# Performance work log

Hardware: AMD Instinct MI355X
Metric: run time of the kernel (lower is better)

The kernel has to match this reference:

```python
import jax, jax.numpy as jnp
import numpy as np

B, IN, OUT = 4096, 1024, 1024
HALF_PI = np.pi / 2.0
TWO_PI = 2.0 * np.pi
# cyclic control-point index table per quadrant (from the torch module)
CPI = jnp.array([[3, 0, 1, 2], [0, 1, 2, 3], [1, 2, 3, 0], [2, 3, 0, 1]], dtype=jnp.int32)
# Catmull-Rom cubic spline basis (4 control points, [t^3,t^2,t,1] monomials)
BASIS = np.array([[-0.5, 1.5, -1.5, 0.5],
                  [1.0, -2.5, 2.0, -0.5],
                  [-0.5, 0.0, 0.5, 0.0],
                  [0.0, 1.0, 0.0, 0.0]], dtype=np.float32)


def setup_inputs() -> dict:
    key = jax.random.key(0)
    k_x, k_p, k_w, k_b = jax.random.split(key, 4)
    x = jax.random.normal(k_x, (B, IN), dtype=jnp.float32)
    phase = jax.random.uniform(k_p, (B,), dtype=jnp.float32) * TWO_PI
    # kaiming_uniform_(a=sqrt(5)) on each (OUT, IN) slice -> bound = 1/sqrt(fan_in)
    bound = 1.0 / np.sqrt(IN)
    weights = jax.random.uniform(k_w, (4, OUT, IN), dtype=jnp.float32, minval=-bound, maxval=bound)
    biases = jax.random.uniform(k_b, (4, OUT), dtype=jnp.float32, minval=-bound, maxval=bound)
    basis = jnp.asarray(BASIS)
    return {"input": x, "phase": phase, "weights": weights, "biases": biases, "basis": basis}


def reference(input, phase, weights, biases, basis):
    # quadrant index q in {0,1,2,3}; same selection as the nested torch.where chain
    q = jnp.clip(jnp.floor(phase / HALF_PI).astype(jnp.int32), 0, 3)          # (B,)
    t = phase / HALF_PI - q.astype(phase.dtype)                                # (B,), in [0,1)
    tt = jnp.stack([t ** 3, t ** 2, t, jnp.ones_like(t)], axis=-1)             # (B,4)
    coeffs = tt @ basis                                                        # (B,4) spline coeffs
    idx = CPI[q]                                                               # (B,4) control-point ids
    # Instead of materializing per-sample (B,OUT,IN) weights, contract input against
    # all 4 control-point matrices (same math: w_b = sum_k c_k W_{idx_k}).
    z = jnp.einsum('bi,coi->bco', input, weights)                              # (B,4,OUT)
    zg = jnp.take_along_axis(z, idx[:, :, None], axis=1)                       # (B,4,OUT)
    bg = biases[idx]                                                           # (B,4,OUT)
    return jnp.einsum('bk,bko->bo', coeffs, zg + bg)                           # (B,OUT)
```

## Files before the change

kernel.cpp:

```cpp
#include <hip/hip_runtime.h>
#include <stdint.h>

#define BATCH   4096
#define IN_DIM  1024
#define OUT_DIM 1024

typedef __bf16 bf16x8 __attribute__((ext_vector_type(8)));
typedef float  f32x4  __attribute__((ext_vector_type(4)));

__device__ __forceinline__ uint16_t f2bf(float f) {
    union { float f; uint32_t u; } v; v.f = f;
    uint32_t u = v.u;
    uint32_t r = (u + 0x7FFFu + ((u >> 16) & 1u)) >> 16;
    return (uint16_t)r;
}

__device__ __forceinline__ float bf2f(uint16_t h) {
    union { uint32_t u; float f; } v; v.u = ((uint32_t)h) << 16;
    return v.f;
}

__global__ __launch_bounds__(256) void prep(
    const float* __restrict__ x, const float* __restrict__ phase,
    const float* __restrict__ basis, const float* __restrict__ W,
    uint16_t* __restrict__ xb, uint16_t* __restrict__ Wb,
    float* __restrict__ alphaWS)
{
    const int bid = blockIdx.x;
    const int tid = threadIdx.x;

    if (bid < BATCH) {
        const int b = bid;
        const float HALF_PI = 1.5707963267948966f;
        float s  = phase[b] / HALF_PI;
        int   q  = (int)floorf(s);
        q = q < 0 ? 0 : (q > 3 ? 3 : q);
        float t  = s - (float)q;
        float t2 = t * t, t3 = t2 * t;

        float coef[4];
#pragma unroll
        for (int j = 0; j < 4; ++j)
            coef[j] = t3 * basis[j] + t2 * basis[4 + j] + t * basis[8 + j] + basis[12 + j];

        if (tid < 4) alphaWS[b * 4 + tid] = coef[(tid - q + 1) & 3];

        float4 xv = ((const float4*)(x + (size_t)b * IN_DIM))[tid];
        ushort4 o;
        o.x = f2bf(xv.x); o.y = f2bf(xv.y); o.z = f2bf(xv.z); o.w = f2bf(xv.w);
        ((ushort4*)(xb + (size_t)b * IN_DIM))[tid] = o;
    } else {
        const int j = bid - BATCH;
        float4 wv = ((const float4*)W)[j * 256 + tid];
        ushort4 o;
        o.x = f2bf(wv.x); o.y = f2bf(wv.y); o.z = f2bf(wv.z); o.w = f2bf(wv.w);
        ((ushort4*)Wb)[j * 256 + tid] = o;
    }
}

__global__ __launch_bounds__(256, 4) void gemm_split(
    const uint16_t* __restrict__ xb, const uint16_t* __restrict__ Wb,
    uint16_t* __restrict__ P)
{
    __shared__ uint16_t As[128 * 64];
    __shared__ uint16_t Bs[128 * 64];

    const int tid  = threadIdx.x;
    const int lane = tid & 63;
    const int wid  = tid >> 6;
    const int wm   = wid >> 1;
    const int wn   = wid & 1;
    const int tileM = blockIdx.x * 128;
    const int tileN = blockIdx.y * 128;
    const int c     = blockIdx.z;

    f32x4 acc[4][4];
#pragma unroll
    for (int mi = 0; mi < 4; ++mi)
#pragma unroll
        for (int ni = 0; ni < 4; ++ni)
            acc[mi][ni] = (f32x4){0.f, 0.f, 0.f, 0.f};

    const int srow = lane >> 3;
    const int gchunk = ((lane & 7) ^ srow) * 8;

    const uint16_t* Ag = xb + (size_t)tileM * 1024;
    const uint16_t* Bg = Wb + ((size_t)c << 20) + (size_t)tileN * 1024;

    const int quad = lane >> 4;
    const int l7   = lane & 7;

    for (int kt = 0; kt < 16; ++kt) {
        const int k0 = kt * 64;
#pragma unroll
        for (int j = 0; j < 4; ++j) {
            const int s = wid * 4 + j;
            const uint16_t* ga = Ag + (size_t)(s * 8 + srow) * 1024 + k0 + gchunk;
            __builtin_amdgcn_global_load_lds(
                (const __attribute__((address_space(1))) void*)ga,
                (__attribute__((address_space(3))) void*)(As + s * 512), 16, 0, 0);
            const uint16_t* gb = Bg + (size_t)(s * 8 + srow) * 1024 + k0 + gchunk;
            __builtin_amdgcn_global_load_lds(
                (const __attribute__((address_space(1))) void*)gb,
                (__attribute__((address_space(3))) void*)(Bs + s * 512), 16, 0, 0);
        }
        __syncthreads();

#pragma unroll
        for (int ks = 0; ks < 2; ++ks) {
            bf16x8 af[4], bfr[4];
#pragma unroll
            for (int mi = 0; mi < 4; ++mi) {
                const int row = wm * 64 + mi * 16 + (lane & 15);
                const int ch  = (ks * 4 + quad) ^ l7;
                af[mi] = *(const bf16x8*)(As + row * 64 + ch * 8);
            }
#pragma unroll
            for (int ni = 0; ni < 4; ++ni) {
                const int row = wn * 64 + ni * 16 + (lane & 15);
                const int ch  = (ks * 4 + quad) ^ l7;
                bfr[ni] = *(const bf16x8*)(Bs + row * 64 + ch * 8);
            }
#pragma unroll
            for (int mi = 0; mi < 4; ++mi)
#pragma unroll
                for (int ni = 0; ni < 4; ++ni)
                    acc[mi][ni] = __builtin_amdgcn_mfma_f32_16x16x32_bf16(
                        af[mi], bfr[ni], acc[mi][ni], 0, 0, 0);
        }
        __syncthreads();
    }

    uint16_t* Pc = P + (size_t)c * (BATCH * (size_t)OUT_DIM);
    const int col0 = tileN + wn * 64 + (lane & 15);
#pragma unroll
    for (int mi = 0; mi < 4; ++mi) {
#pragma unroll
        for (int r = 0; r < 4; ++r) {
            const int m = tileM + wm * 64 + mi * 16 + quad * 4 + r;
#pragma unroll
            for (int ni = 0; ni < 4; ++ni)
                Pc[(size_t)m * OUT_DIM + col0 + ni * 16] = f2bf(acc[mi][ni][r]);
        }
    }
}

__global__ __launch_bounds__(256) void reduce_k(
    const uint16_t* __restrict__ P, const float* __restrict__ alphaWS,
    const float* __restrict__ biases, float* __restrict__ out)
{
    const int m = blockIdx.x;
    const int t = threadIdx.x;
    const size_t stride = (size_t)BATCH * OUT_DIM;

    const float4 al = *(const float4*)(alphaWS + 4 * m);
    float4 r = {0.f, 0.f, 0.f, 0.f};
    const float a[4] = {al.x, al.y, al.z, al.w};
#pragma unroll
    for (int c = 0; c < 4; ++c) {
        ushort4 p = ((const ushort4*)(P + c * stride + (size_t)m * OUT_DIM))[t];
        float4 b  = ((const float4*)(biases + c * OUT_DIM))[t];
        r.x += a[c] * (bf2f(p.x) + b.x);
        r.y += a[c] * (bf2f(p.y) + b.y);
        r.z += a[c] * (bf2f(p.z) + b.z);
        r.w += a[c] * (bf2f(p.w) + b.w);
    }
    ((float4*)(out + (size_t)m * OUT_DIM))[t] = r;
}

extern "C" void kernel_launch(void* const* d_in, const int* in_sizes, int n_in,
                              void* d_out, int out_size, void* d_ws, size_t ws_size,
                              hipStream_t stream)
{
    const float* x       = (const float*)d_in[0];
    const float* phase   = (const float*)d_in[1];
    const float* weights = (const float*)d_in[2];
    const float* biases  = (const float*)d_in[3];
    const float* basis   = (const float*)d_in[4];
    float* out = (float*)d_out;

    uint16_t* xb = (uint16_t*)d_ws;
    uint16_t* Wb = xb + (size_t)BATCH * IN_DIM;
    float* alphaWS = (float*)(Wb + (size_t)4 * OUT_DIM * IN_DIM);
    uint16_t* P = (uint16_t*)(alphaWS + (size_t)BATCH * 4);

    prep<<<2 * BATCH, 256, 0, stream>>>(x, phase, basis, weights, xb, Wb, alphaWS);

    dim3 grid(BATCH / 128, OUT_DIM / 128, 4);
    gemm_split<<<grid, 256, 0, stream>>>(xb, Wb, P);

    reduce_k<<<BATCH, 256, 0, stream>>>(P, alphaWS, biases, out);
}
```

Baseline: 128.7 us.

## Share A tile across two control-point GEMMs per 512-thread block

Each GEMM block now computes two control-point matrices at once with 8 waves. The x tile in LDS is shared, while each wave group reads its own W tile. This cuts redundant global and LDS loads of the input tile by half and halves the grid size. In exchange the blocks are larger, use more LDS, and the grid has fewer blocks, which may affect occupancy and load balance.

```diff
diff --git a/kernel.cpp b/kernel.cpp
--- a/kernel.cpp
+++ b/kernel.cpp
@@ -58,21 +58,22 @@
     }
 }
 
-__global__ __launch_bounds__(256, 4) void gemm_split(
+__global__ __launch_bounds__(512, 4) void gemm_fused2(
     const uint16_t* __restrict__ xb, const uint16_t* __restrict__ Wb,
     uint16_t* __restrict__ P)
 {
     __shared__ uint16_t As[128 * 64];
-    __shared__ uint16_t Bs[128 * 64];
+    __shared__ uint16_t Bs[2][128 * 64];
 
     const int tid  = threadIdx.x;
     const int lane = tid & 63;
     const int wid  = tid >> 6;
-    const int wm   = wid >> 1;
+    const int wc   = wid >> 2;
+    const int wm   = (wid >> 1) & 1;
     const int wn   = wid & 1;
     const int tileM = blockIdx.x * 128;
     const int tileN = blockIdx.y * 128;
-    const int c     = blockIdx.z;
+    const int c0    = blockIdx.z * 2;
 
     f32x4 acc[4][4];
 #pragma unroll
@@ -81,28 +82,32 @@
         for (int ni = 0; ni < 4; ++ni)
             acc[mi][ni] = (f32x4){0.f, 0.f, 0.f, 0.f};
 
-    const int srow = lane >> 3;
+    const int srow   = lane >> 3;
     const int gchunk = ((lane & 7) ^ srow) * 8;
 
-    const uint16_t* Ag = xb + (size_t)tileM * 1024;
-    const uint16_t* Bg = Wb + ((size_t)c << 20) + (size_t)tileN * 1024;
+    const uint16_t* Ag  = xb + (size_t)tileM * 1024;
+    const uint16_t* Bg0 = Wb + ((size_t)c0 << 20) + (size_t)tileN * 1024;
+    const uint16_t* Bg1 = Bg0 + (1u << 20);
 
     const int quad = lane >> 4;
+    const int l15  = lane & 15;
     const int l7   = lane & 7;
 
     for (int kt = 0; kt < 16; ++kt) {
         const int k0 = kt * 64;
 #pragma unroll
-        for (int j = 0; j < 4; ++j) {
-            const int s = wid * 4 + j;
-            const uint16_t* ga = Ag + (size_t)(s * 8 + srow) * 1024 + k0 + gchunk;
+        for (int j = 0; j < 6; ++j) {
+            const int sa  = wid * 6 + j;
+            const int buf = sa >> 4;
+            const int s   = sa & 15;
+            const uint16_t* gsrc =
+                (buf == 0 ? Ag : (buf == 1 ? Bg0 : Bg1))
+                + (size_t)(s * 8 + srow) * 1024 + k0 + gchunk;
+            uint16_t* ldst =
+                (buf == 0 ? As : Bs[buf - 1]) + s * 512;
             __builtin_amdgcn_global_load_lds(
-                (const __attribute__((address_space(1))) void*)ga,
-                (__attribute__((address_space(3))) void*)(As + s * 512), 16, 0, 0);
-            const uint16_t* gb = Bg + (size_t)(s * 8 + srow) * 1024 + k0 + gchunk;
-            __builtin_amdgcn_global_load_lds(
-                (const __attribute__((address_space(1))) void*)gb,
-                (__attribute__((address_space(3))) void*)(Bs + s * 512), 16, 0, 0);
+                (const __attribute__((address_space(1))) void*)gsrc,
+                (__attribute__((address_space(3))) void*)ldst, 16, 0, 0);
         }
         __syncthreads();
 
@@ -111,15 +116,15 @@
             bf16x8 af[4], bfr[4];
 #pragma unroll
             for (int mi = 0; mi < 4; ++mi) {
-                const int row = wm * 64 + mi * 16 + (lane & 15);
+                const int row = wm * 64 + mi * 16 + l15;
                 const int ch  = (ks * 4 + quad) ^ l7;
                 af[mi] = *(const bf16x8*)(As + row * 64 + ch * 8);
             }
 #pragma unroll
             for (int ni = 0; ni < 4; ++ni) {
-                const int row = wn * 64 + ni * 16 + (lane & 15);
+                const int row = wn * 64 + ni * 16 + l15;
                 const int ch  = (ks * 4 + quad) ^ l7;
-                bfr[ni] = *(const bf16x8*)(Bs + row * 64 + ch * 8);
+                bfr[ni] = *(const bf16x8*)(Bs[wc] + row * 64 + ch * 8);
             }
 #pragma unroll
             for (int mi = 0; mi < 4; ++mi)
@@ -131,8 +136,8 @@
         __syncthreads();
     }
 
-    uint16_t* Pc = P + (size_t)c * (BATCH * (size_t)OUT_DIM);
-    const int col0 = tileN + wn * 64 + (lane & 15);
+    uint16_t* Pc = P + (size_t)(c0 + wc) * (BATCH * (size_t)OUT_DIM);
+    const int col0 = tileN + wn * 64 + l15;
 #pragma unroll
     for (int mi = 0; mi < 4; ++mi) {
 #pragma unroll
@@ -186,8 +191,8 @@
 
     prep<<<2 * BATCH, 256, 0, stream>>>(x, phase, basis, weights, xb, Wb, alphaWS);
 
-    dim3 grid(BATCH / 128, OUT_DIM / 128, 4);
-    gemm_split<<<grid, 256, 0, stream>>>(xb, Wb, P);
+    dim3 grid(BATCH / 128, OUT_DIM / 128, 2);
+    gemm_fused2<<<grid, 512, 0, stream>>>(xb, Wb, P);
 
     reduce_k<<<BATCH, 256, 0, stream>>>(P, alphaWS, biases, out);
 }
```

New measurement: 131.9 us. 1.03x slower.
